# Optimization experiments

Hardware: AMD Instinct MI355X
Metric: run time of the kernel (lower is better)

## Reference

```python
import jax, jax.numpy as jnp
import numpy as np

EPS = 1e-5
BOUNDARY = 1.0 - EPS
TEMP = 0.5  # temperature from init_kwargs


def _safe_sqrt(t):
    # sqrt with zero (not inf/nan) gradient at t<=0; matches the analytic clamp
    # in the original custom backward (clamp(z*beta, min=eps)).
    pos = t > 0
    return jnp.where(pos, jnp.sqrt(jnp.where(pos, t, 1.0)), 0.0)


def _poincare_sim(z):
    # z: [2N, D]. Pairwise Poincare distance computed via the matmul identity
    # ||u-v||^2 = ||u||^2 + ||v||^2 - 2 u.v instead of a (2N,2N,D) broadcast.
    raw = jnp.sum(z * z, axis=-1)                      # [2N] unclamped sq norms
    sqc = jnp.clip(raw, 0.0, BOUNDARY)                 # clamped as in forward
    sqdist = jnp.maximum(raw[:, None] + raw[None, :] - 2.0 * (z @ z.T), 0.0)
    x = sqdist / ((1.0 - sqc[:, None]) * (1.0 - sqc[None, :])) * 2.0 + 1.0
    dist = jnp.log(x + _safe_sqrt(x * x - 1.0))        # arcosh(x)
    return 1.0 / (1.0 + dist)                          # Poincare similarity


def setup_inputs() -> dict:
    key = jax.random.key(0)
    k1, k2, k3, k4 = jax.random.split(key, 4)
    N, D = 4096, 8

    def ball(kg, kr):
        g = jax.random.normal(kg, (N, D), dtype=jnp.float32)
        r = jax.random.uniform(kr, (N, 1), dtype=jnp.float32) * 0.85
        return g * r / (jnp.linalg.norm(g, axis=-1, keepdims=True) + 1e-6)

    return {"z_i": ball(k1, k2), "z_j": ball(k3, k4)}


def reference(z_i, z_j):
    N = z_i.shape[0]
    z = jnp.concatenate([z_i, z_j], axis=0)            # [2N, D]
    sim = _poincare_sim(z)                             # [2N, 2N]
    idx = jnp.arange(N)
    # diag(sim, +N) and diag(sim, -N): positive pairs
    positives = jnp.concatenate([sim[idx, idx + N], sim[idx + N, idx]])  # [2N]
    mask = 1.0 - jnp.eye(2 * N, dtype=sim.dtype)       # exclude self-similarity
    denom = jnp.sum(mask * jnp.exp(sim / TEMP), axis=1)  # [2N]
    all_losses = -(positives / TEMP - jnp.log(denom))
    return jnp.sum(all_losses) / (2 * N)
```

## Files before the change

### kernel.cpp

```cpp
#include <hip/hip_runtime.h>
#include <math.h>


#define D 8
#define QS 12
#define TWO_N 8192
#define HALF_N 4096
constexpr int BLOCK   = 256;
constexpr int JC      = 64;
constexpr int GRP     = 4;
constexpr int IBLOCKS = 16;
constexpr int JCHUNKS = 128;
constexpr int NBLK    = IBLOCKS * JCHUNKS;
constexpr int NSEG  = 368;
constexpr int SEG_LO = 1776;
#define BOUNDARY (1.0f - 1e-5f)
#define LN2 0.6931471805599453f

typedef float    f32x2 __attribute__((ext_vector_type(2)));
typedef _Float16 f16x2 __attribute__((ext_vector_type(2)));

__device__ __forceinline__ float frcp(float x)  { return __builtin_amdgcn_rcpf(x); }
__device__ __forceinline__ float fsqrt(float x) { return __builtin_amdgcn_sqrtf(x); }
__device__ __forceinline__ float flog2(float x) { return __builtin_amdgcn_logf(x); }
__device__ __forceinline__ f32x2 splat(float v) { return (f32x2){v, v}; }

__device__ __forceinline__ float dpp_wave_sum(float v) {
    int x;
    x = __builtin_amdgcn_update_dpp(0, __float_as_int(v), 0x111, 0xf, 0xf, false);
    v += __int_as_float(x);
    x = __builtin_amdgcn_update_dpp(0, __float_as_int(v), 0x112, 0xf, 0xf, false);
    v += __int_as_float(x);
    x = __builtin_amdgcn_update_dpp(0, __float_as_int(v), 0x114, 0xf, 0xe, false);
    v += __int_as_float(x);
    x = __builtin_amdgcn_update_dpp(0, __float_as_int(v), 0x118, 0xf, 0xc, false);
    v += __int_as_float(x);
    x = __builtin_amdgcn_update_dpp(0, __float_as_int(v), 0x142, 0xa, 0xf, false);
    v += __int_as_float(x);
    x = __builtin_amdgcn_update_dpp(0, __float_as_int(v), 0x143, 0xc, 0xf, false);
    v += __int_as_float(x);
    return v;
}

__global__ __launch_bounds__(256) void prep_kernel(
    const float* __restrict__ zi, const float* __restrict__ zj,
    float* __restrict__ q, float* __restrict__ out, f16x2* __restrict__ tabh)
{
    const int row = blockIdx.x * 256 + threadIdx.x;
    const float* src = (row < HALF_N) ? (zi + (size_t)row * D)
                                      : (zj + (size_t)(row - HALF_N) * D);
    float4 a = *(const float4*)(src);
    float4 b = *(const float4*)(src + 4);
    float raw = a.x*a.x + a.y*a.y + a.z*a.z + a.w*a.w
              + b.x*b.x + b.y*b.y + b.z*b.z + b.w*b.w;
    float inv = frcp(1.0f - fminf(raw, BOUNDARY));
    float* dst = q + (size_t)row * QS;
    *(float4*)(dst)     = a;
    *(float4*)(dst + 4) = b;
    *(float4*)(dst + 8) = make_float4(inv, inv * raw, 0.0f, 0.0f);
    if (row == 0) out[0] = 0.0f;

    if (row < NSEG) {
        const int m0 = row + SEG_LO;
        const int m1 = m0 + 1;
        float ua_f = __uint_as_float(((unsigned)(m0 >> 4) << 23) | ((unsigned)(m0 & 15) << 19));
        float ub_f = __uint_as_float(((unsigned)(m1 >> 4) << 23) | ((unsigned)(m1 & 15) << 19));
        double ua = (double)ua_f, ub = (double)ub_f;
        double ga = exp(2.0 / (1.0 + log(1.0 + ua + sqrt(ua * (ua + 2.0)))));
        double gb = exp(2.0 / (1.0 + log(1.0 + ub + sqrt(ub * (ub + 2.0)))));
        double sl = (gb - ga) / (ub - ua);
        double ic = ga - sl * ua;
        tabh[row] = (f16x2){(_Float16)(float)sl, (_Float16)(float)ic};
    }
}

struct QCol { float4 a; float4 b; float2 c; };

__device__ __forceinline__ float lut1(float u, const f16x2* __restrict__ tab)
{
    int t = (int)(__float_as_uint(u) >> 19) - SEG_LO;
    t = (t < 0) ? 0 : t;
    t = (t > NSEG - 1) ? NSEG - 1 : t;
    f16x2 si = tab[t];
    return fmaf((float)si.x, u, (float)si.y);
}

template<int MODE>
__device__ __forceinline__ f32x2 tile_loop(
    const float* __restrict__ q, const f16x2* __restrict__ stab, int jbase,
    const f32x2* __restrict__ s2, f32x2 t8, f32x2 t9, f32x2 m4,
    int irow0, int irow1)
{
    f32x2 accE = splat(0.0f), accO = splat(0.0f);
    #pragma unroll 2
    for (int g = 0; g < JC / GRP; ++g) {
        QCol qg[GRP];
        #pragma unroll
        for (int c = 0; c < GRP; ++c) {
            const float* qp = q + (size_t)(jbase + g * GRP + c) * QS;
            qg[c].a = *(const float4*)(qp);
            qg[c].b = *(const float4*)(qp + 4);
            qg[c].c = *(const float2*)(qp + 8);
        }
        #pragma unroll
        for (int c = 0; c < GRP; ++c) {
            f32x2 S = splat(0.0f);
            S = __builtin_elementwise_fma(s2[0], splat(qg[c].a.x), S);
            S = __builtin_elementwise_fma(s2[1], splat(qg[c].a.y), S);
            S = __builtin_elementwise_fma(s2[2], splat(qg[c].a.z), S);
            S = __builtin_elementwise_fma(s2[3], splat(qg[c].a.w), S);
            S = __builtin_elementwise_fma(s2[4], splat(qg[c].b.x), S);
            S = __builtin_elementwise_fma(s2[5], splat(qg[c].b.y), S);
            S = __builtin_elementwise_fma(s2[6], splat(qg[c].b.z), S);
            S = __builtin_elementwise_fma(s2[7], splat(qg[c].b.w), S);

            f32x2 A = t8 * splat(qg[c].c.x);
            A = __builtin_elementwise_fma(t9, splat(qg[c].c.y), A);

            f32x2 msel;
            if (MODE == 0) {
                msel = m4;
            } else {
                const float nm = -4.0f * qg[c].c.x;
                if (MODE == 1) {
                    msel = splat(nm);
                } else {
                    const int j = jbase + g * GRP + c;
                    msel.x = (j > irow0) ? m4.x : nm;
                    msel.y = (j > irow1) ? m4.y : nm;
                }
            }
            f32x2 u = __builtin_elementwise_fma(S, msel, A);
            u = __builtin_elementwise_max(u, splat(0.0f));
            if (c & 1) { accO.x += lut1(u.x, stab); accO.y += lut1(u.y, stab); }
            else       { accE.x += lut1(u.x, stab); accE.y += lut1(u.y, stab); }
        }
    }
    return accE + accO;
}

__global__ __launch_bounds__(BLOCK, 8) void pair_kernel(
    const float* __restrict__ q, const f16x2* __restrict__ gtabh,
    float* __restrict__ part)
{
    __shared__ alignas(16) f16x2 stab[NSEG];

    const int tid   = threadIdx.x;
    const int ib    = blockIdx.x >> 7;
    const int jc    = blockIdx.x & (JCHUNKS - 1);
    const int ibase = ib * 512;
    const int jbase = jc * JC;

    if (tid < NSEG / 4)
        ((float4*)stab)[tid] = ((const float4*)gtabh)[tid];

    const int irow0 = ibase + tid;
    const int irow1 = irow0 + 256;
    f32x2 s2[8], t8, t9, m4;
    {
        const float* q0 = q + (size_t)irow0 * QS;
        const float* q1 = q + (size_t)irow1 * QS;
        float4 a0 = *(const float4*)(q0), b0 = *(const float4*)(q0 + 4);
        float2 c0 = *(const float2*)(q0 + 8);
        float4 a1 = *(const float4*)(q1), b1 = *(const float4*)(q1 + 4);
        float2 c1 = *(const float2*)(q1 + 8);
        s2[0] = (f32x2){a0.x, a1.x}; s2[1] = (f32x2){a0.y, a1.y};
        s2[2] = (f32x2){a0.z, a1.z}; s2[3] = (f32x2){a0.w, a1.w};
        s2[4] = (f32x2){b0.x, b1.x}; s2[5] = (f32x2){b0.y, b1.y};
        s2[6] = (f32x2){b0.z, b1.z}; s2[7] = (f32x2){b0.w, b1.w};
        t8 = (f32x2){2.0f * c0.y, 2.0f * c1.y};
        t9 = (f32x2){2.0f * c0.x, 2.0f * c1.x};
        m4 = (f32x2){-4.0f * c0.x, -4.0f * c1.x};
    }
    __syncthreads();

    f32x2 acc;
    if (jbase >= ibase + 512)
        acc = tile_loop<0>(q, stab, jbase, s2, t8, t9, m4, irow0, irow1);
    else if (jbase + JC <= ibase)
        acc = tile_loop<1>(q, stab, jbase, s2, t8, t9, m4, irow0, irow1);
    else
        acc = tile_loop<2>(q, stab, jbase, s2, t8, t9, m4, irow0, irow1);

    part[(size_t)jc * TWO_N + irow0] = acc.x;
    part[(size_t)jc * TWO_N + irow1] = acc.y;
}

__global__ __launch_bounds__(256) void reduce_kernel(
    const float* __restrict__ zi, const float* __restrict__ zj,
    const float* __restrict__ part, const f16x2* __restrict__ gtabh,
    float* __restrict__ out)
{
    __shared__ float swred[4];
    const int tid = threadIdx.x;
    const int i   = blockIdx.x * 256 + tid;

    float rs = 0.0f;
    {
        const float* pp = part + i;
        #pragma unroll 8
        for (int c = 0; c < JCHUNKS; ++c) rs += pp[(size_t)c * TWO_N];
    }

    const int base = (i < HALF_N) ? i : (i - HALF_N);
    const float* pa = (i < HALF_N) ? (zi + (size_t)base * D) : (zj + (size_t)base * D);
    const float* pb = (i < HALF_N) ? (zj + (size_t)base * D) : (zi + (size_t)base * D);
    float4 a0 = *(const float4*)(pa), a1 = *(const float4*)(pa + 4);
    float4 b0 = *(const float4*)(pb), b1 = *(const float4*)(pb + 4);
    float rawa = a0.x*a0.x + a0.y*a0.y + a0.z*a0.z + a0.w*a0.w
               + a1.x*a1.x + a1.y*a1.y + a1.z*a1.z + a1.w*a1.w;
    float rawb = b0.x*b0.x + b0.y*b0.y + b0.z*b0.z + b0.w*b0.w
               + b1.x*b1.x + b1.y*b1.y + b1.z*b1.z + b1.w*b1.w;
    float dot  = a0.x*b0.x + a0.y*b0.y + a0.z*b0.z + a0.w*b0.w
               + a1.x*b1.x + a1.y*b1.y + a1.z*b1.z + a1.w*b1.w;
    float sqd  = fmaxf(rawa + rawb - 2.0f * dot, 0.0f);
    float inva = frcp(1.0f - fminf(rawa, BOUNDARY));
    float invb = frcp(1.0f - fminf(rawb, BOUNDARY));
    float x    = fmaf(2.0f * sqd, inva * invb, 1.0f);
    float t    = fmaf(x, x, -1.0f);
    float s    = fsqrt(fmaxf(t, 0.0f));
    float dist = flog2(x + s) * LN2;
    float sim  = frcp(1.0f + dist);

    float cy = inva * rawa;
    float A  = (2.0f * cy) * inva;
    A = fmaf(2.0f * inva, cy, A);
    float us = fmaxf(fmaf(rawa, -4.0f * inva, A), 0.0f);
    int tt = (int)(__float_as_uint(us) >> 19) - SEG_LO;
    tt = (tt < 0) ? 0 : tt;
    tt = (tt > NSEG - 1) ? NSEG - 1 : tt;
    f16x2 sih = gtabh[tt];
    float es = fmaf((float)sih.x, us, (float)sih.y);

    float denomv = rs - es;
    float dlog = flog2(denomv) * LN2;
    float term = -(2.0f * sim - dlog);

    float ws = dpp_wave_sum(term);
    if ((tid & 63) == 63) swred[tid >> 6] = ws;
    __syncthreads();
    if (tid == 0)
        atomicAdd(out, (swred[0] + swred[1] + swred[2] + swred[3])
                           * (1.0f / (float)TWO_N));
}

extern "C" void kernel_launch(void* const* d_in, const int* in_sizes, int n_in,
                              void* d_out, int out_size, void* d_ws, size_t ws_size,
                              hipStream_t stream) {
    const float* zi = (const float*)d_in[0];
    const float* zj = (const float*)d_in[1];

    float* q    = (float*)d_ws;
    f16x2* tabh = (f16x2*)(q + (size_t)TWO_N * QS);
    float* part = (float*)((char*)tabh + 2048);

    prep_kernel<<<TWO_N / 256, 256, 0, stream>>>(zi, zj, q, (float*)d_out, tabh);

    pair_kernel<<<NBLK, BLOCK, 0, stream>>>(q, tabh, part);

    reduce_kernel<<<TWO_N / 256, 256, 0, stream>>>(zi, zj, part, tabh, (float*)d_out);
}
```

Before: 88.06 us.

## Build exp-similarity LUT per block in fp32 and replace index clamps with value clamps

The slope/intercept table is no longer built in double precision in the prep kernel. Each pair and reduce block now computes it in shared memory using fast fp32 hardware log/exp/rcp, which removes the slow fp64 transcendentals and the global table round-trip. The per-element integer index clamps in the LUT lookup become a float min/max clamp on u. The reduce kernel moves to 128-thread blocks. The cost is redundant table construction in all 2048 pair blocks, which adds transcendental work before the main loop, and table entries that differ slightly in accuracy.

After: 87.89 us. Within noise of the previous version (-0.2%).

```diff
diff --git a/kernel.cpp b/kernel.cpp
--- a/kernel.cpp
+++ b/kernel.cpp
@@ -1,5 +1,4 @@
 #include <hip/hip_runtime.h>
-#include <math.h>
 
 
 #define D 8
@@ -15,7 +14,10 @@
 constexpr int NSEG  = 368;
 constexpr int SEG_LO = 1776;
 #define BOUNDARY (1.0f - 1e-5f)
-#define LN2 0.6931471805599453f
+#define LN2   0.6931471805599453f
+#define LOG2E 1.4426950408889634f
+#define UMIN  1.52587890625e-05f
+#define UMAX  127.0f
 
 typedef float    f32x2 __attribute__((ext_vector_type(2)));
 typedef _Float16 f16x2 __attribute__((ext_vector_type(2)));
@@ -23,6 +25,7 @@
 __device__ __forceinline__ float frcp(float x)  { return __builtin_amdgcn_rcpf(x); }
 __device__ __forceinline__ float fsqrt(float x) { return __builtin_amdgcn_sqrtf(x); }
 __device__ __forceinline__ float flog2(float x) { return __builtin_amdgcn_logf(x); }
+__device__ __forceinline__ float fexp2(float x) { return __builtin_amdgcn_exp2f(x); }
 __device__ __forceinline__ f32x2 splat(float v) { return (f32x2){v, v}; }
 
 __device__ __forceinline__ float dpp_wave_sum(float v) {
@@ -42,35 +45,23 @@
     return v;
 }
 
-__global__ __launch_bounds__(256) void prep_kernel(
-    const float* __restrict__ zi, const float* __restrict__ zj,
-    float* __restrict__ q, float* __restrict__ out, f16x2* __restrict__ tabh)
-{
-    const int row = blockIdx.x * 256 + threadIdx.x;
-    const float* src = (row < HALF_N) ? (zi + (size_t)row * D)
-                                      : (zj + (size_t)(row - HALF_N) * D);
-    float4 a = *(const float4*)(src);
-    float4 b = *(const float4*)(src + 4);
-    float raw = a.x*a.x + a.y*a.y + a.z*a.z + a.w*a.w
-              + b.x*b.x + b.y*b.y + b.z*b.z + b.w*b.w;
-    float inv = frcp(1.0f - fminf(raw, BOUNDARY));
-    float* dst = q + (size_t)row * QS;
-    *(float4*)(dst)     = a;
-    *(float4*)(dst + 4) = b;
-    *(float4*)(dst + 8) = make_float4(inv, inv * raw, 0.0f, 0.0f);
-    if (row == 0) out[0] = 0.0f;
-
-    if (row < NSEG) {
-        const int m0 = row + SEG_LO;
+__device__ __forceinline__ float gfun(float u) {
+    float y = 1.0f + u + fsqrt(fmaf(u, u, 2.0f * u));
+    float d = flog2(y) * LN2;
+    return fexp2(2.0f * LOG2E * frcp(1.0f + d));
+}
+
+template<int NTHREADS>
+__device__ __forceinline__ void build_stab(f16x2* stab, int tid) {
+    for (int e = tid; e < NSEG; e += NTHREADS) {
+        const int m0 = e + SEG_LO;
         const int m1 = m0 + 1;
-        float ua_f = __uint_as_float(((unsigned)(m0 >> 4) << 23) | ((unsigned)(m0 & 15) << 19));
-        float ub_f = __uint_as_float(((unsigned)(m1 >> 4) << 23) | ((unsigned)(m1 & 15) << 19));
-        double ua = (double)ua_f, ub = (double)ub_f;
-        double ga = exp(2.0 / (1.0 + log(1.0 + ua + sqrt(ua * (ua + 2.0)))));
-        double gb = exp(2.0 / (1.0 + log(1.0 + ub + sqrt(ub * (ub + 2.0)))));
-        double sl = (gb - ga) / (ub - ua);
-        double ic = ga - sl * ua;
-        tabh[row] = (f16x2){(_Float16)(float)sl, (_Float16)(float)ic};
+        float ua = __uint_as_float(((unsigned)(m0 >> 4) << 23) | ((unsigned)(m0 & 15) << 19));
+        float ub = __uint_as_float(((unsigned)(m1 >> 4) << 23) | ((unsigned)(m1 & 15) << 19));
+        float ga = gfun(ua), gb = gfun(ub);
+        float sl = (gb - ga) / (ub - ua);
+        float ic = fmaf(-sl, ua, ga);
+        stab[e] = (f16x2){(_Float16)sl, (_Float16)ic};
     }
 }
 
@@ -79,8 +70,6 @@
 __device__ __forceinline__ float lut1(float u, const f16x2* __restrict__ tab)
 {
     int t = (int)(__float_as_uint(u) >> 19) - SEG_LO;
-    t = (t < 0) ? 0 : t;
-    t = (t > NSEG - 1) ? NSEG - 1 : t;
     f16x2 si = tab[t];
     return fmaf((float)si.x, u, (float)si.y);
 }
@@ -131,7 +120,8 @@
                 }
             }
             f32x2 u = __builtin_elementwise_fma(S, msel, A);
-            u = __builtin_elementwise_max(u, splat(0.0f));
+            u = __builtin_elementwise_max(u, splat(UMIN));
+            u = __builtin_elementwise_min(u, splat(UMAX));
             if (c & 1) { accO.x += lut1(u.x, stab); accO.y += lut1(u.y, stab); }
             else       { accE.x += lut1(u.x, stab); accE.y += lut1(u.y, stab); }
         }
@@ -139,9 +129,27 @@
     return accE + accO;
 }
 
+__global__ __launch_bounds__(256) void prep_kernel(
+    const float* __restrict__ zi, const float* __restrict__ zj,
+    float* __restrict__ q, float* __restrict__ out)
+{
+    const int row = blockIdx.x * 256 + threadIdx.x;
+    const float* src = (row < HALF_N) ? (zi + (size_t)row * D)
+                                      : (zj + (size_t)(row - HALF_N) * D);
+    float4 a = *(const float4*)(src);
+    float4 b = *(const float4*)(src + 4);
+    float raw = a.x*a.x + a.y*a.y + a.z*a.z + a.w*a.w
+              + b.x*b.x + b.y*b.y + b.z*b.z + b.w*b.w;
+    float inv = frcp(1.0f - fminf(raw, BOUNDARY));
+    float* dst = q + (size_t)row * QS;
+    *(float4*)(dst)     = a;
+    *(float4*)(dst + 4) = b;
+    *(float4*)(dst + 8) = make_float4(inv, inv * raw, 0.0f, 0.0f);
+    if (row == 0) out[0] = 0.0f;
+}
+
 __global__ __launch_bounds__(BLOCK, 8) void pair_kernel(
-    const float* __restrict__ q, const f16x2* __restrict__ gtabh,
-    float* __restrict__ part)
+    const float* __restrict__ q, float* __restrict__ part)
 {
     __shared__ alignas(16) f16x2 stab[NSEG];
 
@@ -151,8 +159,7 @@
     const int ibase = ib * 512;
     const int jbase = jc * JC;
 
-    if (tid < NSEG / 4)
-        ((float4*)stab)[tid] = ((const float4*)gtabh)[tid];
+    build_stab<BLOCK>(stab, tid);
 
     const int irow0 = ibase + tid;
     const int irow1 = irow0 + 256;
@@ -186,14 +193,16 @@
     part[(size_t)jc * TWO_N + irow1] = acc.y;
 }
 
-__global__ __launch_bounds__(256) void reduce_kernel(
+__global__ __launch_bounds__(128) void reduce_kernel(
     const float* __restrict__ zi, const float* __restrict__ zj,
-    const float* __restrict__ part, const f16x2* __restrict__ gtabh,
-    float* __restrict__ out)
-{
-    __shared__ float swred[4];
+    const float* __restrict__ part, float* __restrict__ out)
+{
+    __shared__ alignas(16) f16x2 stab[NSEG];
+    __shared__ float swred[2];
     const int tid = threadIdx.x;
-    const int i   = blockIdx.x * 256 + tid;
+    const int i   = blockIdx.x * 128 + tid;
+
+    build_stab<128>(stab, tid);
 
     float rs = 0.0f;
     {
@@ -222,15 +231,14 @@
     float dist = flog2(x + s) * LN2;
     float sim  = frcp(1.0f + dist);
 
+    __syncthreads();
+
     float cy = inva * rawa;
     float A  = (2.0f * cy) * inva;
     A = fmaf(2.0f * inva, cy, A);
-    float us = fmaxf(fmaf(rawa, -4.0f * inva, A), 0.0f);
-    int tt = (int)(__float_as_uint(us) >> 19) - SEG_LO;
-    tt = (tt < 0) ? 0 : tt;
-    tt = (tt > NSEG - 1) ? NSEG - 1 : tt;
-    f16x2 sih = gtabh[tt];
-    float es = fmaf((float)sih.x, us, (float)sih.y);
+    float us = fmaf(rawa, -4.0f * inva, A);
+    us = fminf(fmaxf(us, UMIN), UMAX);
+    float es = lut1(us, stab);
 
     float denomv = rs - es;
     float dlog = flog2(denomv) * LN2;
@@ -240,8 +248,7 @@
     if ((tid & 63) == 63) swred[tid >> 6] = ws;
     __syncthreads();
     if (tid == 0)
-        atomicAdd(out, (swred[0] + swred[1] + swred[2] + swred[3])
-                           * (1.0f / (float)TWO_N));
+        atomicAdd(out, (swred[0] + swred[1]) * (1.0f / (float)TWO_N));
 }
 
 extern "C" void kernel_launch(void* const* d_in, const int* in_sizes, int n_in,
@@ -251,12 +258,11 @@
     const float* zj = (const float*)d_in[1];
 
     float* q    = (float*)d_ws;
-    f16x2* tabh = (f16x2*)(q + (size_t)TWO_N * QS);
-    float* part = (float*)((char*)tabh + 2048);
-
-    prep_kernel<<<TWO_N / 256, 256, 0, stream>>>(zi, zj, q, (float*)d_out, tabh);
-
-    pair_kernel<<<NBLK, BLOCK, 0, stream>>>(q, tabh, part);
-
-    reduce_kernel<<<TWO_N / 256, 256, 0, stream>>>(zi, zj, part, tabh, (float*)d_out);
-}
+    float* part = q + (size_t)TWO_N * QS;
+
+    prep_kernel<<<TWO_N / 256, 256, 0, stream>>>(zi, zj, q, (float*)d_out);
+
+    pair_kernel<<<NBLK, BLOCK, 0, stream>>>(q, part);
+
+    reduce_kernel<<<TWO_N / 128, 128, 0, stream>>>(zi, zj, part, (float*)d_out);
+}
```
